# Optimization experiments

Hardware: AMD Instinct MI355X
Metric: run time of the kernel (lower is better)

Reference implementation:

```python
import jax, jax.numpy as jnp
import numpy as np

B, G, C = 512, 8192, 6
REGION_NUM = 1024


def setup_inputs() -> dict:
    key = jax.random.key(0)
    k1, k2, k3 = jax.random.split(key, 3)
    # points clustered at ~5cm scale so some fall inside the gripper box
    group_points = jax.random.normal(k1, (B, G, C), jnp.float32) * 0.05
    group_index = jax.random.randint(k2, (B, G), 0, 100000, dtype=jnp.int32)
    grasp = jax.random.normal(k3, (B, 7), jnp.float32) * 0.05
    return {
        "group_points": group_points,
        "group_index": group_index,
        "grasp": grasp,
        "widths": jnp.float32(0.08),
        "height": jnp.float32(0.04),
        "depths": jnp.float32(0.06),
        "region_num": REGION_NUM,
    }


def _normalize_fix(v, fallback):
    # normalize rows of [B,3]; rows with zero norm are replaced by `fallback`
    eps = 1e-12
    n = jnp.linalg.norm(v, axis=1)
    v = v / (n + eps)[:, None]
    return jnp.where((n == 0.0)[:, None], jnp.asarray(fallback, v.dtype), v)


def _transform(group_points, grasp):
    # Per-grasp frame construction + rotation of group points into gripper frame.
    center = grasp[:, 0:3]            # [B,3]
    axis_y = grasp[:, 3:6]            # [B,3]
    angle = grasp[:, 6]               # [B]
    c, s = jnp.cos(angle), jnp.sin(angle)
    zero, one = jnp.zeros_like(c), jnp.ones_like(c)
    # rotation about y by angle: [[c,0,-s],[0,1,0],[s,0,c]]
    R1 = jnp.stack([c, zero, -s, zero, one, zero, s, zero, c], axis=1).reshape(-1, 3, 3)
    axis_y = _normalize_fix(axis_y, [0.0, 1.0, 0.0])
    axis_x = jnp.stack([axis_y[:, 1], -axis_y[:, 0], zero], axis=1)
    axis_x = _normalize_fix(axis_x, [1.0, 0.0, 0.0])
    axis_z = jnp.cross(axis_x, axis_y)
    nz = jnp.linalg.norm(axis_z, axis=1)
    axis_z = axis_z / jnp.where(nz == 0.0, 1.0, nz)[:, None]
    axis_z = jnp.where((nz == 0.0)[:, None], jnp.asarray([0.0, 0.0, 1.0], axis_z.dtype), axis_z)
    M = jnp.stack([axis_x, axis_y, axis_z], axis=2) @ R1   # columns are axes, [B,3,3]
    approach = _normalize_fix(M[:, :, 0], [1.0, 0.0, 0.0])
    minor = jnp.cross(approach, axis_y)
    Mrows = jnp.stack([approach, axis_y, minor], axis=1)    # rows = frame axes, [B,3,3]
    # pcs_t[b,n,:] = Mrows[b] @ (p[b,n] - center[b])
    pcs_t = jnp.einsum('bij,bnj->bni', Mrows, group_points[:, :, :3] - center[:, None, :])
    return pcs_t


def reference(group_points, group_index, grasp, widths, height, depths, region_num):
    pcs_t = _transform(group_points, grasp)              # [B,G,3]
    x_lim, y_lim, z_lim = depths / 2, widths / 2, height / 2
    x, y, z = pcs_t[..., 0], pcs_t[..., 1], pcs_t[..., 2]
    mask = (x > 0) & (x < x_lim) & (y > -y_lim) & (y < y_lim) & (z > -z_lim) & (z < z_lim)  # [B,G]
    count = mask.sum(axis=1)                             # [B]
    # stable sort: indices of in-box points first, in original order
    order = jnp.argsort(jnp.where(mask, 0, 1).astype(jnp.int32), axis=1, stable=True)
    j = jnp.arange(region_num)
    # deterministic compaction: take first region_num hits; wrap (sample with
    # replacement) when fewer than region_num hits are available
    pos = j[None, :] % jnp.maximum(count, 1)[:, None]
    idx = jnp.take_along_axis(order, pos, axis=1)        # [B,region_num]
    valid = count > 5                                    # [B]
    pc = jnp.concatenate(
        [jnp.take_along_axis(pcs_t, idx[:, :, None], axis=1),
         jnp.take_along_axis(group_points[:, :, 3:], idx[:, :, None], axis=1)], axis=-1)
    gripper_pc = jnp.where(valid[:, None, None], pc, -1.0)             # [B,region_num,6]
    gripper_pc_index = jnp.where(valid[:, None], idx, -1)              # [B,region_num]
    gripper_pc_index_inall = jnp.where(
        valid[:, None], jnp.take_along_axis(group_index, idx, axis=1), -1)
    true_mask = valid.astype(jnp.float32)                              # [B]
    return gripper_pc, gripper_pc_index, gripper_pc_index_inall, true_mask
```

## Files before the change

### kernel.cpp

```cpp
#include <hip/hip_runtime.h>


__device__ __forceinline__ float fm(float a, float b) { return __fmul_rn(a, b); }
__device__ __forceinline__ float fa(float a, float b) { return __fadd_rn(a, b); }
__device__ __forceinline__ float fs(float a, float b) { return __fsub_rn(a, b); }
__device__ __forceinline__ float fd(float a, float b) { return __fdiv_rn(a, b); }

struct Xform {
    float r0x, r0y, r0z;
    float r1x, r1y, r1z;
    float r2x, r2y, r2z;
    float cx, cy, cz;
};

__device__ Xform compute_xform(const float* __restrict__ gr) {
    Xform X;
    X.cx = gr[0]; X.cy = gr[1]; X.cz = gr[2];
    float vx = gr[3], vy = gr[4], vz = gr[5];
    float angle = gr[6];
    float c = (float)cos((double)angle);
    float s = (float)sin((double)angle);

    float n  = __fsqrt_rn(fa(fa(fm(vx, vx), fm(vy, vy)), fm(vz, vz)));
    float dn = fa(n, 1e-12f);
    float ayx = fd(vx, dn), ayy = fd(vy, dn), ayz = fd(vz, dn);
    if (n == 0.0f) { ayx = 0.0f; ayy = 1.0f; ayz = 0.0f; }

    float bx = ayy, by = -ayx, bz = 0.0f;
    float n2  = __fsqrt_rn(fa(fa(fm(bx, bx), fm(by, by)), fm(bz, bz)));
    float dn2 = fa(n2, 1e-12f);
    float axx = fd(bx, dn2), axy = fd(by, dn2), axz = fd(bz, dn2);
    if (n2 == 0.0f) { axx = 1.0f; axy = 0.0f; axz = 0.0f; }

    float zx = fs(fm(axy, ayz), fm(axz, ayy));
    float zy = fs(fm(axz, ayx), fm(axx, ayz));
    float zz = fs(fm(axx, ayy), fm(axy, ayx));
    float nz = __fsqrt_rn(fa(fa(fm(zx, zx), fm(zy, zy)), fm(zz, zz)));
    float dz = (nz == 0.0f) ? 1.0f : nz;
    zx = fd(zx, dz); zy = fd(zy, dz); zz = fd(zz, dz);
    if (nz == 0.0f) { zx = 0.0f; zy = 0.0f; zz = 1.0f; }

    float px = fa(fm(axx, c), fm(zx, s));
    float py = fa(fm(axy, c), fm(zy, s));
    float pz = fa(fm(axz, c), fm(zz, s));
    float n3  = __fsqrt_rn(fa(fa(fm(px, px), fm(py, py)), fm(pz, pz)));
    float dn3 = fa(n3, 1e-12f);
    float apx = fd(px, dn3), apy = fd(py, dn3), apz = fd(pz, dn3);
    if (n3 == 0.0f) { apx = 1.0f; apy = 0.0f; apz = 0.0f; }

    float mx = fs(fm(apy, ayz), fm(apz, ayy));
    float my = fs(fm(apz, ayx), fm(apx, ayz));
    float mz = fs(fm(apx, ayy), fm(apy, ayx));

    X.r0x = apx; X.r0y = apy; X.r0z = apz;
    X.r1x = ayx; X.r1y = ayy; X.r1z = ayz;
    X.r2x = mx;  X.r2y = my;  X.r2z = mz;
    return X;
}

__device__ __forceinline__ void transform_point(const Xform& X,
                                                float px, float py, float pz,
                                                float& x, float& y, float& z) {
    float dx = fs(px, X.cx), dy = fs(py, X.cy), dz = fs(pz, X.cz);
    x = fa(fa(fm(X.r0x, dx), fm(X.r0y, dy)), fm(X.r0z, dz));
    y = fa(fa(fm(X.r1x, dx), fm(X.r1y, dy)), fm(X.r1z, dz));
    z = fa(fa(fm(X.r2x, dx), fm(X.r2y, dy)), fm(X.r2z, dz));
}

#define NTHREADS 1024
#define NWAVES (NTHREADS / 64)

extern "C" __global__ void __launch_bounds__(NTHREADS)
gripper_kernel(const float* __restrict__ gp,
               const int*   __restrict__ gidx,
               const float* __restrict__ grasp,
               const float* __restrict__ widths_p,
               const float* __restrict__ height_p,
               const float* __restrict__ depths_p,
               float* __restrict__ out,
               int B, int G, int RN) {
    const int b    = blockIdx.x;
    const int tid  = threadIdx.x;
    const int lane = tid & 63;
    const int wave = tid >> 6;

    extern __shared__ int s_idx[];
    __shared__ int s_cnt[NWAVES];
    __shared__ int s_total;

    const Xform X = compute_xform(grasp + (size_t)b * 7);

    const float x_lim = fm(*depths_p, 0.5f);
    const float y_lim = fm(*widths_p, 0.5f);
    const float z_lim = fm(*height_p, 0.5f);

    if (tid == 0) s_total = 0;
    __syncthreads();

    const float* __restrict__ gpb = gp + (size_t)b * G * 6;

    for (int base = 0; base < G; base += NTHREADS) {
        int g = base + tid;
        const float* p = gpb + (size_t)g * 6;
        float x, y, z;
        transform_point(X, p[0], p[1], p[2], x, y, z);
        bool m = (x > 0.0f) & (x < x_lim) & (y > -y_lim) & (y < y_lim) &
                 (z > -z_lim) & (z < z_lim);

        unsigned long long bal = __ballot(m);
        if (lane == 0) s_cnt[wave] = __popcll(bal);
        __syncthreads();

        int off = s_total;
        #pragma unroll
        for (int w = 0; w < NWAVES; ++w)
            if (w < wave) off += s_cnt[w];
        int pos = off + __popcll(bal & ((1ull << lane) - 1ull));
        if (m && pos < RN) s_idx[pos] = g;
        __syncthreads();

        if (tid == 0) {
            int t = 0;
            #pragma unroll
            for (int w = 0; w < NWAVES; ++w) t += s_cnt[w];
            s_total += t;
        }
        __syncthreads();
    }

    const int count = s_total;

    float* __restrict__ out0 = out;
    float* __restrict__ out1 = out + (size_t)B * RN * 6;
    float* __restrict__ out2 = out1 + (size_t)B * RN;
    float* __restrict__ out3 = out2 + (size_t)B * RN;

    if (count > 5) {
        const int m = count < RN ? count : RN;
        for (int j = tid; j < RN; j += NTHREADS) {
            int i = s_idx[j % m];
            const float* p = gpb + (size_t)i * 6;
            float x, y, z;
            transform_point(X, p[0], p[1], p[2], x, y, z);
            size_t o0 = ((size_t)b * RN + j) * 6;
            out0[o0 + 0] = x;
            out0[o0 + 1] = y;
            out0[o0 + 2] = z;
            out0[o0 + 3] = p[3];
            out0[o0 + 4] = p[4];
            out0[o0 + 5] = p[5];
            out1[(size_t)b * RN + j] = (float)i;
            out2[(size_t)b * RN + j] = (float)gidx[(size_t)b * G + i];
        }
        if (tid == 0) out3[b] = 1.0f;
    } else {
        for (int j = tid; j < RN; j += NTHREADS) {
            size_t o0 = ((size_t)b * RN + j) * 6;
            #pragma unroll
            for (int k = 0; k < 6; ++k) out0[o0 + k] = -1.0f;
            out1[(size_t)b * RN + j] = -1.0f;
            out2[(size_t)b * RN + j] = -1.0f;
        }
        if (tid == 0) out3[b] = 0.0f;
    }
}

extern "C" void kernel_launch(void* const* d_in, const int* in_sizes, int n_in,
                              void* d_out, int out_size, void* d_ws, size_t ws_size,
                              hipStream_t stream) {
    const float* gp     = (const float*)d_in[0];
    const int*   gidx   = (const int*)d_in[1];
    const float* grasp  = (const float*)d_in[2];
    const float* widths = (const float*)d_in[3];
    const float* height = (const float*)d_in[4];
    const float* depths = (const float*)d_in[5];
    float* out = (float*)d_out;

    const int B  = in_sizes[2] / 7;
    const int G  = in_sizes[1] / B;
    const int RN = (out_size / B - 1) / 8;

    const size_t smem = (size_t)RN * sizeof(int);
    gripper_kernel<<<B, NTHREADS, smem, stream>>>(gp, gidx, grasp, widths,
                                                  height, depths, out, B, G, RN);
}
```

Before: 179.1 us.

## Precompute grasp frames in separate kernel and cut compaction barriers

```diff
diff --git a/kernel.cpp b/kernel.cpp
--- a/kernel.cpp
+++ b/kernel.cpp
@@ -6,16 +6,13 @@
 __device__ __forceinline__ float fs(float a, float b) { return __fsub_rn(a, b); }
 __device__ __forceinline__ float fd(float a, float b) { return __fdiv_rn(a, b); }
 
-struct Xform {
-    float r0x, r0y, r0z;
-    float r1x, r1y, r1z;
-    float r2x, r2y, r2z;
-    float cx, cy, cz;
-};
+extern "C" __global__ void xform_kernel(const float* __restrict__ grasp,
+                                        float* __restrict__ xf, int B) {
+    int b = blockIdx.x * blockDim.x + threadIdx.x;
+    if (b >= B) return;
+    const float* gr = grasp + (size_t)b * 7;
 
-__device__ Xform compute_xform(const float* __restrict__ gr) {
-    Xform X;
-    X.cx = gr[0]; X.cy = gr[1]; X.cz = gr[2];
+    float cx = gr[0], cy = gr[1], cz = gr[2];
     float vx = gr[3], vy = gr[4], vz = gr[5];
     float angle = gr[6];
     float c = (float)cos((double)angle);
@@ -26,10 +23,10 @@
     float ayx = fd(vx, dn), ayy = fd(vy, dn), ayz = fd(vz, dn);
     if (n == 0.0f) { ayx = 0.0f; ayy = 1.0f; ayz = 0.0f; }
 
-    float bx = ayy, by = -ayx, bz = 0.0f;
-    float n2  = __fsqrt_rn(fa(fa(fm(bx, bx), fm(by, by)), fm(bz, bz)));
+    float bx = ayy, by = -ayx;
+    float n2  = __fsqrt_rn(fa(fa(fm(bx, bx), fm(by, by)), 0.0f));
     float dn2 = fa(n2, 1e-12f);
-    float axx = fd(bx, dn2), axy = fd(by, dn2), axz = fd(bz, dn2);
+    float axx = fd(bx, dn2), axy = fd(by, dn2), axz = fd(0.0f, dn2);
     if (n2 == 0.0f) { axx = 1.0f; axy = 0.0f; axz = 0.0f; }
 
     float zx = fs(fm(axy, ayz), fm(axz, ayy));
@@ -52,19 +49,11 @@
     float my = fs(fm(apz, ayx), fm(apx, ayz));
     float mz = fs(fm(apx, ayy), fm(apy, ayx));
 
-    X.r0x = apx; X.r0y = apy; X.r0z = apz;
-    X.r1x = ayx; X.r1y = ayy; X.r1z = ayz;
-    X.r2x = mx;  X.r2y = my;  X.r2z = mz;
-    return X;
-}
-
-__device__ __forceinline__ void transform_point(const Xform& X,
-                                                float px, float py, float pz,
-                                                float& x, float& y, float& z) {
-    float dx = fs(px, X.cx), dy = fs(py, X.cy), dz = fs(pz, X.cz);
-    x = fa(fa(fm(X.r0x, dx), fm(X.r0y, dy)), fm(X.r0z, dz));
-    y = fa(fa(fm(X.r1x, dx), fm(X.r1y, dy)), fm(X.r1z, dz));
-    z = fa(fa(fm(X.r2x, dx), fm(X.r2y, dy)), fm(X.r2z, dz));
+    float* o = xf + (size_t)b * 12;
+    o[0] = apx; o[1] = apy; o[2]  = apz;
+    o[3] = ayx; o[4] = ayy; o[5]  = ayz;
+    o[6] = mx;  o[7] = my;  o[8]  = mz;
+    o[9] = cx;  o[10] = cy; o[11] = cz;
 }
 
 #define NTHREADS 1024
@@ -73,7 +62,7 @@
 extern "C" __global__ void __launch_bounds__(NTHREADS)
 gripper_kernel(const float* __restrict__ gp,
                const int*   __restrict__ gidx,
-               const float* __restrict__ grasp,
+               const float* __restrict__ xf,
                const float* __restrict__ widths_p,
                const float* __restrict__ height_p,
                const float* __restrict__ depths_p,
@@ -85,50 +74,53 @@
     const int wave = tid >> 6;
 
     extern __shared__ int s_idx[];
-    __shared__ int s_cnt[NWAVES];
-    __shared__ int s_total;
+    __shared__ int s_cnt[2][NWAVES];
 
-    const Xform X = compute_xform(grasp + (size_t)b * 7);
+    const float4 q0 = *(const float4*)(xf + (size_t)b * 12 + 0);
+    const float4 q1 = *(const float4*)(xf + (size_t)b * 12 + 4);
+    const float4 q2 = *(const float4*)(xf + (size_t)b * 12 + 8);
+    const float r0x = q0.x, r0y = q0.y, r0z = q0.z;
+    const float r1x = q0.w, r1y = q1.x, r1z = q1.y;
+    const float r2x = q1.z, r2y = q1.w, r2z = q2.x;
+    const float cx  = q2.y, cy  = q2.z, cz  = q2.w;
 
     const float x_lim = fm(*depths_p, 0.5f);
     const float y_lim = fm(*widths_p, 0.5f);
     const float z_lim = fm(*height_p, 0.5f);
 
-    if (tid == 0) s_total = 0;
+    const float* __restrict__ gpb = gp + (size_t)b * G * 6;
+
+    int running = 0;
+    const int niter = G / NTHREADS;
+    for (int it = 0; it < niter; ++it) {
+        const int g = it * NTHREADS + tid;
+        const float2 l0 = *(const float2*)(gpb + (size_t)g * 6);
+        const float2 l1 = *(const float2*)(gpb + (size_t)g * 6 + 2);
+        const float dx = fs(l0.x, cx), dy = fs(l0.y, cy), dz = fs(l1.x, cz);
+        const float x = fa(fa(fm(r0x, dx), fm(r0y, dy)), fm(r0z, dz));
+        const float y = fa(fa(fm(r1x, dx), fm(r1y, dy)), fm(r1z, dz));
+        const float z = fa(fa(fm(r2x, dx), fm(r2y, dy)), fm(r2z, dz));
+        const bool m = (x > 0.0f) & (x < x_lim) & (y > -y_lim) & (y < y_lim) &
+                       (z > -z_lim) & (z < z_lim);
+
+        const unsigned long long bal = __ballot(m);
+        if (lane == 0) s_cnt[it & 1][wave] = __popcll(bal);
+        __syncthreads();
+
+        int off = running, tot = 0;
+        #pragma unroll
+        for (int w = 0; w < NWAVES; ++w) {
+            const int cw = s_cnt[it & 1][w];
+            if (w < wave) off += cw;
+            tot += cw;
+        }
+        const int pos = off + __popcll(bal & ((1ull << lane) - 1ull));
+        if (m && pos < RN) s_idx[pos] = g;
+        running += tot;
+    }
     __syncthreads();
 
-    const float* __restrict__ gpb = gp + (size_t)b * G * 6;
-
-    for (int base = 0; base < G; base += NTHREADS) {
-        int g = base + tid;
-        const float* p = gpb + (size_t)g * 6;
-        float x, y, z;
-        transform_point(X, p[0], p[1], p[2], x, y, z);
-        bool m = (x > 0.0f) & (x < x_lim) & (y > -y_lim) & (y < y_lim) &
-                 (z > -z_lim) & (z < z_lim);
-
-        unsigned long long bal = __ballot(m);
-        if (lane == 0) s_cnt[wave] = __popcll(bal);
-        __syncthreads();
-
-        int off = s_total;
-        #pragma unroll
-        for (int w = 0; w < NWAVES; ++w)
-            if (w < wave) off += s_cnt[w];
-        int pos = off + __popcll(bal & ((1ull << lane) - 1ull));
-        if (m && pos < RN) s_idx[pos] = g;
-        __syncthreads();
-
-        if (tid == 0) {
-            int t = 0;
-            #pragma unroll
-            for (int w = 0; w < NWAVES; ++w) t += s_cnt[w];
-            s_total += t;
-        }
-        __syncthreads();
-    }
-
-    const int count = s_total;
+    const int count = running;
 
     float* __restrict__ out0 = out;
     float* __restrict__ out1 = out + (size_t)B * RN * 6;
@@ -138,26 +130,30 @@
     if (count > 5) {
         const int m = count < RN ? count : RN;
         for (int j = tid; j < RN; j += NTHREADS) {
-            int i = s_idx[j % m];
+            const int i = s_idx[j % m];
             const float* p = gpb + (size_t)i * 6;
-            float x, y, z;
-            transform_point(X, p[0], p[1], p[2], x, y, z);
-            size_t o0 = ((size_t)b * RN + j) * 6;
-            out0[o0 + 0] = x;
-            out0[o0 + 1] = y;
-            out0[o0 + 2] = z;
-            out0[o0 + 3] = p[3];
-            out0[o0 + 4] = p[4];
-            out0[o0 + 5] = p[5];
+            const float2 l0 = *(const float2*)(p);
+            const float2 l1 = *(const float2*)(p + 2);
+            const float2 l2 = *(const float2*)(p + 4);
+            const float dx = fs(l0.x, cx), dy = fs(l0.y, cy), dz = fs(l1.x, cz);
+            const float x = fa(fa(fm(r0x, dx), fm(r0y, dy)), fm(r0z, dz));
+            const float y = fa(fa(fm(r1x, dx), fm(r1y, dy)), fm(r1z, dz));
+            const float z = fa(fa(fm(r2x, dx), fm(r2y, dy)), fm(r2z, dz));
+            float* o = out0 + ((size_t)b * RN + j) * 6;
+            *(float2*)(o + 0) = make_float2(x, y);
+            *(float2*)(o + 2) = make_float2(z, l1.y);
+            *(float2*)(o + 4) = l2;
             out1[(size_t)b * RN + j] = (float)i;
             out2[(size_t)b * RN + j] = (float)gidx[(size_t)b * G + i];
         }
         if (tid == 0) out3[b] = 1.0f;
     } else {
         for (int j = tid; j < RN; j += NTHREADS) {
-            size_t o0 = ((size_t)b * RN + j) * 6;
-            #pragma unroll
-            for (int k = 0; k < 6; ++k) out0[o0 + k] = -1.0f;
+            float* o = out0 + ((size_t)b * RN + j) * 6;
+            const float2 neg = make_float2(-1.0f, -1.0f);
+            *(float2*)(o + 0) = neg;
+            *(float2*)(o + 2) = neg;
+            *(float2*)(o + 4) = neg;
             out1[(size_t)b * RN + j] = -1.0f;
             out2[(size_t)b * RN + j] = -1.0f;
         }
@@ -175,12 +171,15 @@
     const float* height = (const float*)d_in[4];
     const float* depths = (const float*)d_in[5];
     float* out = (float*)d_out;
+    float* xf  = (float*)d_ws;
 
     const int B  = in_sizes[2] / 7;
     const int G  = in_sizes[1] / B;
     const int RN = (out_size / B - 1) / 8;
 
+    xform_kernel<<<(B + 255) / 256, 256, 0, stream>>>(grasp, xf, B);
+
     const size_t smem = (size_t)RN * sizeof(int);
-    gripper_kernel<<<B, NTHREADS, smem, stream>>>(gp, gidx, grasp, widths,
+    gripper_kernel<<<B, NTHREADS, smem, stream>>>(gp, gidx, xf, widths,
                                                   height, depths, out, B, G, RN);
 }
```

Result: no change. 180.4 us (+0.7%).
